# Performance work log

Hardware: AMD Instinct MI355X
Metric: run time of the kernel (lower is better)

The kernel has to match this reference:

```python
import jax, jax.numpy as jnp
import numpy as np

N_NODES = 50000
N_EDGES = 800000
NFEAT, NHID, NCLASS = 512, 64, 40


def setup_inputs() -> dict:
    key = jax.random.key(0)
    ks = jax.random.split(key, 10)
    x = jax.random.normal(ks[0], (N_NODES, NFEAT), dtype=jnp.float32)
    edge_weight = jax.random.uniform(ks[1], (N_EDGES,), dtype=jnp.float32)
    W1 = jax.random.normal(ks[2], (NFEAT, NHID), dtype=jnp.float32) / np.sqrt(NFEAT)
    b1 = jnp.zeros((NHID,), dtype=jnp.float32)
    W2 = jax.random.normal(ks[3], (NHID, NHID), dtype=jnp.float32) / np.sqrt(NHID)
    b2 = jnp.zeros((NHID,), dtype=jnp.float32)
    W3 = jax.random.normal(ks[4], (NHID, NCLASS), dtype=jnp.float32) / np.sqrt(NHID)
    b3 = jnp.zeros((NCLASS,), dtype=jnp.float32)
    row = jax.random.randint(ks[5], (N_EDGES,), 0, N_NODES, dtype=jnp.int32)
    col = jax.random.randint(ks[6], (N_EDGES,), 0, N_NODES, dtype=jnp.int32)
    return {"x": x, "edge_weight": edge_weight, "W1": W1, "b1": b1,
            "W2": W2, "b2": b2, "W3": W3, "b3": b3, "row": row, "col": col}


def _gcn_layer(h, W, b, row, col, ew):
    # support = h @ W + b ; out = spmm(adj, support)
    support = h @ W + b                      # [N, dout]
    msg = support[col] * ew[:, None]         # gather + scale, [E, dout]
    return jax.ops.segment_sum(msg, row, num_segments=N_NODES)


def reference(x, edge_weight, W1, b1, W2, b2, W3, b3, row, col):
    h = jax.nn.relu(_gcn_layer(x, W1, b1, row, col, edge_weight))
    # dropout: eval mode -> identity
    h = _gcn_layer(h, W2, b2, row, col, edge_weight)
    h = _gcn_layer(h, W3, b3, row, col, edge_weight)
    return jax.nn.log_softmax(h, axis=1)
```

## Files before the change

kernel.cpp:

```cpp
#include <hip/hip_runtime.h>
#include <hip/hip_bf16.h>

#define NNODES 50000
#define NEDGES 800000
#define NFEAT  512
#define NHID   64
#define NCLASS 40

#define CAP 48
#define CNTSTRIDE 16
#define FILL_BLOCKS ((NEDGES + 255) / 256)
#define GEMM1_BLOCKS ((NNODES + 63) / 64)

typedef __attribute__((ext_vector_type(8))) short short8;
typedef __attribute__((ext_vector_type(4))) float floatx4;

static __device__ __forceinline__ unsigned short f2bf(float f) {
    union { float f; unsigned u; } v; v.f = f;
    const unsigned r = v.u + 0x7fffu + ((v.u >> 16) & 1u);
    return (unsigned short)(r >> 16);
}
static __device__ __forceinline__ float bf2f(unsigned u) {
    union { unsigned u; float f; } v; v.u = u << 16;
    return v.f;
}

template<int NCB, int NVALID>
static __device__ __forceinline__ void convW_body(
    const float* __restrict__ W, unsigned short* __restrict__ wb, int idx) {
    const int lane = idx & 63;
    const int cb   = (idx >> 6) % NCB;
    const int kb   = idx / (64 * NCB);
    const int q = lane >> 4, m = lane & 15;
    const int c = cb * 16 + m;
    short8 v;
    #pragma unroll
    for (int j = 0; j < 8; ++j)
        v[j] = (c < NVALID)
             ? (short)f2bf(W[(size_t)(kb * 32 + q * 8 + j) * NVALID + c])
             : (short)0;
    *(short8*)(wb + (size_t)idx * 8) = v;
}

__global__ __launch_bounds__(256) void conv_kernel(
    const float* __restrict__ W1, unsigned short* __restrict__ wb1,
    const float* __restrict__ W2, unsigned short* __restrict__ wb2,
    const float* __restrict__ W3, unsigned short* __restrict__ wb3,
    int4* __restrict__ cnt4) {
    const int blk = blockIdx.x;
    const int tid = threadIdx.x;
    if (blk < 16) {
        convW_body<4, 64>(W1, wb1, blk * 256 + tid);
    } else if (blk < 18) {
        convW_body<4, 64>(W2, wb2, (blk - 16) * 256 + tid);
    } else if (blk < 20) {
        const int idx = (blk - 18) * 256 + tid;
        if (idx < 2 * 3 * 64) convW_body<3, 40>(W3, wb3, idx);
    } else {
        const int i = (blk - 20) * 256 + tid;
        if (i < NNODES * CNTSTRIDE / 4) cnt4[i] = make_int4(0, 0, 0, 0);
    }
}

__global__ __launch_bounds__(256) void bucket_gemm1_kernel(
    const int* __restrict__ row, const int* __restrict__ col,
    const float* __restrict__ ew, int* __restrict__ cnt,
    unsigned* __restrict__ bucket,
    const float* __restrict__ x, const unsigned short* __restrict__ wb,
    const float* __restrict__ b, unsigned short* __restrict__ outb) {
    const int blk = blockIdx.x;
    const int tid = threadIdx.x;
    const int g = blk / 5;
    const int r = blk % 5;

    if (r != 0) {
        const int e = (4 * g + r - 1) * 256 + tid;
        if (e >= NEDGES) return;
        const int rr = row[e];
        const int pos = atomicAdd(&cnt[rr * CNTSTRIDE], 1);
        if (pos < CAP)
            bucket[(size_t)rr * CAP + pos] =
                (unsigned)col[e] | ((unsigned)f2bf(ew[e]) << 16);
        return;
    }

    const int lane = tid & 63;
    const int wid  = tid >> 6;
    const int q = lane >> 4, m = lane & 15;

    const int rowbase = g * 64 + wid * 16;
    int rload = rowbase + m;
    if (rload >= NNODES) rload = NNODES - 1;
    const float* xp = x + (size_t)rload * NFEAT + q * 8;

    floatx4 acc[4];
    #pragma unroll
    for (int cb = 0; cb < 4; ++cb) acc[cb] = (floatx4)0.f;

    for (int kb = 0; kb < 16; ++kb) {
        const float4 a0 = *(const float4*)(xp + kb * 32);
        const float4 a1 = *(const float4*)(xp + kb * 32 + 4);
        short8 afrag;
        afrag[0] = (short)f2bf(a0.x); afrag[1] = (short)f2bf(a0.y);
        afrag[2] = (short)f2bf(a0.z); afrag[3] = (short)f2bf(a0.w);
        afrag[4] = (short)f2bf(a1.x); afrag[5] = (short)f2bf(a1.y);
        afrag[6] = (short)f2bf(a1.z); afrag[7] = (short)f2bf(a1.w);

        const unsigned short* wp = wb + ((size_t)(kb * 4) * 64 + lane) * 8;
        #pragma unroll
        for (int cb = 0; cb < 4; ++cb) {
            const short8 bfrag = *(const short8*)(wp + (size_t)cb * 64 * 8);
            acc[cb] = __builtin_amdgcn_mfma_f32_16x16x32_bf16(
                afrag, bfrag, acc[cb], 0, 0, 0);
        }
    }

    const int orow = rowbase + q * 4;
    #pragma unroll
    for (int cb = 0; cb < 4; ++cb) {
        const int c = cb * 16 + m;
        const float bias = b[c];
        #pragma unroll
        for (int i = 0; i < 4; ++i) {
            const int rr2 = orow + i;
            if (rr2 < NNODES)
                outb[(size_t)rr2 * NHID + c] = f2bf(acc[cb][i] + bias);
        }
    }
}

template<bool RELU, int NCB, int NOUT>
__global__ __launch_bounds__(256) void spmm_gemm_kernel(
    const unsigned short* __restrict__ supb, const unsigned* __restrict__ bucket,
    const int* __restrict__ cnt, const unsigned short* __restrict__ wb,
    const float* __restrict__ bias, unsigned short* __restrict__ outb) {
    __shared__ unsigned short ht[4 * 72];

    const int tid  = threadIdx.x;
    const int wid  = tid >> 6;
    const int lane = tid & 63;
    const int half = lane >> 5;
    const int fp   = lane & 31;
    const int n    = blockIdx.x * 4 + wid;

    float a0 = 0.f, a1 = 0.f;
    if (n < NNODES) {
        int deg = cnt[n * CNTSTRIDE];
        if (deg > CAP) deg = CAP;
        const unsigned* ep = bucket + (size_t)n * CAP;
        for (int i = half; i < deg; i += 16) {
            unsigned eb[8], vb[8];
            #pragma unroll
            for (int j = 0; j < 8; ++j) {
                const int idx = i + 2 * j;
                eb[j] = (idx < deg) ? ep[idx] : 0u;
            }
            #pragma unroll
            for (int j = 0; j < 8; ++j)
                vb[j] = *(const unsigned*)(supb + (size_t)(eb[j] & 0xffffu) * NHID + fp * 2);
            #pragma unroll
            for (int j = 0; j < 8; ++j) {
                const float w = bf2f(eb[j] >> 16);
                a0 += w * bf2f(vb[j] & 0xffffu);
                a1 += w * bf2f(vb[j] >> 16);
            }
        }
    }
    a0 += __shfl_xor(a0, 32);
    a1 += __shfl_xor(a1, 32);
    if (RELU) { a0 = fmaxf(a0, 0.f); a1 = fmaxf(a1, 0.f); }
    if (half == 0)
        *(unsigned*)&ht[wid * 72 + fp * 2] =
            (unsigned)f2bf(a0) | ((unsigned)f2bf(a1) << 16);
    __syncthreads();

    if (wid != 0) return;
    const int q = lane >> 4, m = lane & 15;
    const unsigned short* hp = &ht[(m & 3) * 72 + q * 8];

    floatx4 acc[NCB];
    #pragma unroll
    for (int cb = 0; cb < NCB; ++cb) acc[cb] = (floatx4)0.f;

    #pragma unroll
    for (int kb = 0; kb < 2; ++kb) {
        const short8 afrag = *(const short8*)(hp + kb * 32);
        const unsigned short* wp = wb + ((size_t)(kb * NCB) * 64 + lane) * 8;
        #pragma unroll
        for (int cb = 0; cb < NCB; ++cb) {
            const short8 bfrag = *(const short8*)(wp + (size_t)cb * 64 * 8);
            acc[cb] = __builtin_amdgcn_mfma_f32_16x16x32_bf16(
                afrag, bfrag, acc[cb], 0, 0, 0);
        }
    }

    if (q != 0) return;
    #pragma unroll
    for (int cb = 0; cb < NCB; ++cb) {
        const int c = cb * 16 + m;
        if (c >= NOUT) continue;
        const float bv = bias[c];
        #pragma unroll
        for (int i = 0; i < 4; ++i) {
            const int r = blockIdx.x * 4 + i;
            if (r < NNODES)
                outb[(size_t)r * NOUT + c] = f2bf(acc[cb][i] + bv);
        }
    }
}

__global__ __launch_bounds__(256) void spmm_bf40_lsm_kernel(
    const unsigned short* __restrict__ supb, const unsigned* __restrict__ bucket,
    const int* __restrict__ cnt, float* __restrict__ out) {
    const int f = threadIdx.x & 63;
    const int n = blockIdx.x * 4 + (threadIdx.x >> 6);
    if (n >= NNODES) return;
    int deg = cnt[n * CNTSTRIDE];
    if (deg > CAP) deg = CAP;
    const unsigned* ep = bucket + (size_t)n * CAP;
    float acc = 0.f;
    if (f < NCLASS) {
        for (int i = 0; i < deg; i += 8) {
            unsigned eb[8]; float vb[8];
            #pragma unroll
            for (int j = 0; j < 8; ++j) {
                const int idx = i + j;
                eb[j] = (idx < deg) ? ep[idx] : 0u;
            }
            #pragma unroll
            for (int j = 0; j < 8; ++j)
                vb[j] = bf2f(supb[(size_t)(eb[j] & 0xffffu) * NCLASS + f]);
            #pragma unroll
            for (int j = 0; j < 8; ++j)
                acc += vb[j] * bf2f(eb[j] >> 16);
        }
    }
    float m = (f < NCLASS) ? acc : -1e30f;
    #pragma unroll
    for (int o = 32; o > 0; o >>= 1) m = fmaxf(m, __shfl_xor(m, o));
    float ex = (f < NCLASS) ? __expf(acc - m) : 0.f;
    #pragma unroll
    for (int o = 32; o > 0; o >>= 1) ex += __shfl_xor(ex, o);
    const float ls = __logf(ex) + m;
    if (f < NCLASS) out[(size_t)n * NCLASS + f] = acc - ls;
}

extern "C" void kernel_launch(void* const* d_in, const int* in_sizes, int n_in,
                              void* d_out, int out_size, void* d_ws, size_t ws_size,
                              hipStream_t stream) {
    const float* x  = (const float*)d_in[0];
    const float* ew = (const float*)d_in[1];
    const float* W1 = (const float*)d_in[2];
    const float* b1 = (const float*)d_in[3];
    const float* W2 = (const float*)d_in[4];
    const float* b2 = (const float*)d_in[5];
    const float* W3 = (const float*)d_in[6];
    const float* b3 = (const float*)d_in[7];
    const int* row  = (const int*)d_in[8];
    const int* col  = (const int*)d_in[9];
    float* out = (float*)d_out;

    const size_t n64 = (size_t)NNODES * NHID;
    const size_t n40 = (size_t)NNODES * NCLASS;
    unsigned* bucket = (unsigned*)d_ws;
    int* cnt = (int*)(bucket + (size_t)NNODES * CAP);
    unsigned short* S1 = (unsigned short*)(cnt + (size_t)NNODES * CNTSTRIDE);
    unsigned short* S2 = S1 + n64;
    unsigned short* S3 = S2 + n64;
    unsigned short* wb1 = S3 + n40;
    unsigned short* wb2 = wb1 + 16 * 4 * 64 * 8;
    unsigned short* wb3 = wb2 + 2 * 4 * 64 * 8;

    const int nodeBlocks = (NNODES + 3) / 4;

    conv_kernel<<<820, 256, 0, stream>>>(W1, wb1, W2, wb2, W3, wb3, (int4*)cnt);

    bucket_gemm1_kernel<<<GEMM1_BLOCKS + FILL_BLOCKS, 256, 0, stream>>>(
        row, col, ew, cnt, bucket, x, wb1, b1, S1);

    spmm_gemm_kernel<true, 4, 64><<<nodeBlocks, 256, 0, stream>>>(
        S1, bucket, cnt, wb2, b2, S2);

    spmm_gemm_kernel<false, 3, 40><<<nodeBlocks, 256, 0, stream>>>(
        S2, bucket, cnt, wb3, b3, S3);

    spmm_bf40_lsm_kernel<<<nodeBlocks, 256, 0, stream>>>(S3, bucket, cnt, out);
}
```

Measured before the change: 300.1 us.

## Split GEMM1 K dimension across wave pairs and batch x loads

The first-layer GEMM block now covers 32 rows instead of 64, with two waves each handling half of the 512-wide K dimension for 16 rows. The partial sums are combined through shared memory. Loads of x are batched four k-steps at a time to raise memory-level parallelism. The bucket-fill interleave changes from 4:1 to 2:1 so the block count matches the smaller GEMM tiles. This doubles the number of GEMM blocks to improve latency hiding on the bandwidth-bound x stream, at the cost of a __syncthreads and a shared-memory reduction.

```diff
diff --git a/kernel.cpp b/kernel.cpp
--- a/kernel.cpp
+++ b/kernel.cpp
@@ -10,7 +10,7 @@
 #define CAP 48
 #define CNTSTRIDE 16
 #define FILL_BLOCKS ((NEDGES + 255) / 256)
-#define GEMM1_BLOCKS ((NNODES + 63) / 64)
+#define GEMM1_BLOCKS ((NNODES + 31) / 32)
 
 typedef __attribute__((ext_vector_type(8))) short short8;
 typedef __attribute__((ext_vector_type(4))) float floatx4;
@@ -70,11 +70,11 @@
     const float* __restrict__ b, unsigned short* __restrict__ outb) {
     const int blk = blockIdx.x;
     const int tid = threadIdx.x;
-    const int g = blk / 5;
-    const int r = blk % 5;
+    const int g = blk / 3;
+    const int r = blk % 3;
 
     if (r != 0) {
-        const int e = (4 * g + r - 1) * 256 + tid;
+        const int e = (2 * g + r - 1) * 256 + tid;
         if (e >= NEDGES) return;
         const int rr = row[e];
         const int pos = atomicAdd(&cnt[rr * CNTSTRIDE], 1);
@@ -84,36 +84,59 @@
         return;
     }
 
+    __shared__ float red[2][16][64];
+
     const int lane = tid & 63;
     const int wid  = tid >> 6;
+    const int p  = wid >> 1;
+    const int kh = wid & 1;
     const int q = lane >> 4, m = lane & 15;
 
-    const int rowbase = g * 64 + wid * 16;
+    const int rowbase = g * 32 + p * 16;
     int rload = rowbase + m;
     if (rload >= NNODES) rload = NNODES - 1;
-    const float* xp = x + (size_t)rload * NFEAT + q * 8;
+    const float* xp = x + (size_t)rload * NFEAT + kh * 256 + q * 8;
 
     floatx4 acc[4];
     #pragma unroll
     for (int cb = 0; cb < 4; ++cb) acc[cb] = (floatx4)0.f;
 
-    for (int kb = 0; kb < 16; ++kb) {
-        const float4 a0 = *(const float4*)(xp + kb * 32);
-        const float4 a1 = *(const float4*)(xp + kb * 32 + 4);
-        short8 afrag;
-        afrag[0] = (short)f2bf(a0.x); afrag[1] = (short)f2bf(a0.y);
-        afrag[2] = (short)f2bf(a0.z); afrag[3] = (short)f2bf(a0.w);
-        afrag[4] = (short)f2bf(a1.x); afrag[5] = (short)f2bf(a1.y);
-        afrag[6] = (short)f2bf(a1.z); afrag[7] = (short)f2bf(a1.w);
-
-        const unsigned short* wp = wb + ((size_t)(kb * 4) * 64 + lane) * 8;
-        #pragma unroll
-        for (int cb = 0; cb < 4; ++cb) {
-            const short8 bfrag = *(const short8*)(wp + (size_t)cb * 64 * 8);
-            acc[cb] = __builtin_amdgcn_mfma_f32_16x16x32_bf16(
-                afrag, bfrag, acc[cb], 0, 0, 0);
-        }
-    }
+    #pragma unroll
+    for (int kc = 0; kc < 2; ++kc) {
+        float4 a0[4], a1[4];
+        #pragma unroll
+        for (int u = 0; u < 4; ++u) {
+            a0[u] = *(const float4*)(xp + (kc * 4 + u) * 32);
+            a1[u] = *(const float4*)(xp + (kc * 4 + u) * 32 + 4);
+        }
+        #pragma unroll
+        for (int u = 0; u < 4; ++u) {
+            short8 afrag;
+            afrag[0] = (short)f2bf(a0[u].x); afrag[1] = (short)f2bf(a0[u].y);
+            afrag[2] = (short)f2bf(a0[u].z); afrag[3] = (short)f2bf(a0[u].w);
+            afrag[4] = (short)f2bf(a1[u].x); afrag[5] = (short)f2bf(a1[u].y);
+            afrag[6] = (short)f2bf(a1[u].z); afrag[7] = (short)f2bf(a1[u].w);
+
+            const int kbg = kh * 8 + kc * 4 + u;
+            const unsigned short* wp = wb + ((size_t)(kbg * 4) * 64 + lane) * 8;
+            #pragma unroll
+            for (int cb = 0; cb < 4; ++cb) {
+                const short8 bfrag = *(const short8*)(wp + (size_t)cb * 64 * 8);
+                acc[cb] = __builtin_amdgcn_mfma_f32_16x16x32_bf16(
+                    afrag, bfrag, acc[cb], 0, 0, 0);
+            }
+        }
+    }
+
+    if (kh == 1) {
+        #pragma unroll
+        for (int cb = 0; cb < 4; ++cb)
+            #pragma unroll
+            for (int i = 0; i < 4; ++i)
+                red[p][q * 4 + i][cb * 16 + m] = acc[cb][i];
+    }
+    __syncthreads();
+    if (kh == 1) return;
 
     const int orow = rowbase + q * 4;
     #pragma unroll
@@ -124,7 +147,8 @@
         for (int i = 0; i < 4; ++i) {
             const int rr2 = orow + i;
             if (rr2 < NNODES)
-                outb[(size_t)rr2 * NHID + c] = f2bf(acc[cb][i] + bias);
+                outb[(size_t)rr2 * NHID + c] =
+                    f2bf(acc[cb][i] + red[p][q * 4 + i][c] + bias);
         }
     }
 }
@@ -275,7 +299,7 @@
 
     conv_kernel<<<820, 256, 0, stream>>>(W1, wb1, W2, wb2, W3, wb3, (int4*)cnt);
 
-    bucket_gemm1_kernel<<<GEMM1_BLOCKS + FILL_BLOCKS, 256, 0, stream>>>(
+    bucket_gemm1_kernel<<<3 * GEMM1_BLOCKS, 256, 0, stream>>>(
         row, col, ew, cnt, bucket, x, wb1, b1, S1);
 
     spmm_gemm_kernel<true, 4, 64><<<nodeBlocks, 256, 0, stream>>>(
```

New measurement: 295.7 us. About the same (-1.5%).
